# Kernel optimization log

Hardware: AMD Instinct MI355X
Metric: run time of the kernel (lower is better)

## Reference

```python
import jax, jax.numpy as jnp
import numpy as np

N_NODES = 100000
N_EDGES = 250000
EMB = 300
LAYERS = 5
BN_EPS = 1e-5


def setup_inputs() -> dict:
    key = jax.random.key(0)
    ks = jax.random.split(key, 16)
    inp = {
        "x": jax.random.randint(ks[0], (N_NODES, 2), 0, 3, dtype=jnp.int64) if jax.config.jax_enable_x64 else jax.random.randint(ks[0], (N_NODES, 2), 0, 3, dtype=jnp.int32),
        "edge_index": jax.random.randint(ks[1], (2, N_EDGES), 0, N_NODES, dtype=jnp.int32),
        "edge_attr": jax.random.randint(ks[2], (N_EDGES, 2), 0, 3, dtype=jnp.int32),
        "atom_emb1": jax.random.normal(ks[3], (120, EMB), jnp.float32) * 0.1,
        "atom_emb2": jax.random.normal(ks[4], (3, EMB), jnp.float32) * 0.1,
        "edge_emb1": jax.random.normal(ks[5], (LAYERS, 6, EMB), jnp.float32) * 0.1,
        "edge_emb2": jax.random.normal(ks[6], (LAYERS, 3, EMB), jnp.float32) * 0.1,
        "W1": jax.random.normal(ks[7], (LAYERS, EMB, 2 * EMB), jnp.float32) * (1.0 / np.sqrt(EMB)),
        "b1": jnp.zeros((LAYERS, 2 * EMB), jnp.float32),
        "W2": jax.random.normal(ks[8], (LAYERS, 2 * EMB, EMB), jnp.float32) * (1.0 / np.sqrt(2 * EMB)),
        "b2": jnp.zeros((LAYERS, EMB), jnp.float32),
        "gamma": jnp.ones((LAYERS, EMB), jnp.float32),
        "beta": jnp.zeros((LAYERS, EMB), jnp.float32),
    }
    return inp


def reference(x, edge_index, edge_attr, atom_emb1, atom_emb2, edge_emb1, edge_emb2,
              W1, b1, W2, b2, gamma, beta):
    N = x.shape[0]
    L = W1.shape[0]
    # AtomEncoder: sum of per-feature embeddings
    h = atom_emb1[x[:, 0]] + atom_emb2[x[:, 1]]  # [N, D]
    # add self loops (attr = (4, 0)); PyG: messages flow src=row0 -> dst=row1
    sl = jnp.arange(N, dtype=edge_index.dtype)
    src = jnp.concatenate([edge_index[0], sl])
    dst = jnp.concatenate([edge_index[1], sl])
    ea0 = jnp.concatenate([edge_attr[:, 0], jnp.full((N,), 4, edge_attr.dtype)])
    ea1 = jnp.concatenate([edge_attr[:, 1], jnp.zeros((N,), edge_attr.dtype)])
    for l in range(L):
        e = edge_emb1[l][ea0] + edge_emb2[l][ea1]           # [E+N, D]
        msg = h[src] + e                                     # gather + add
        agg = jax.ops.segment_sum(msg, dst, num_segments=N)  # scatter-add
        hmid = jax.nn.relu(agg @ W1[l] + b1[l])
        hout = hmid @ W2[l] + b2[l]
        mean = hout.mean(axis=0)
        var = hout.var(axis=0)
        hbn = (hout - mean) * jax.lax.rsqrt(var + BN_EPS) * gamma[l] + beta[l]
        h = hbn if l == L - 1 else jax.nn.relu(hbn)          # dropout ratio 0
    return h
```

## Files before the change

### kernel.cpp

```cpp
#include <hip/hip_runtime.h>
#include <hip/hip_bf16.h>

#define N_NODESC 100000
#define N_EDGESC 250000
#define EMB 300
#define LD 304
#define LD4 76
#define LAYERS 5
#define BN_EPS 1e-5f

#define K1 320
#define N1 640
#define K2 640
#define N2 384

#define NB_SCAN 391

typedef __attribute__((ext_vector_type(8))) short short8;
typedef __attribute__((ext_vector_type(4))) float f32x4;

#define GLOAD16(g, l) __builtin_amdgcn_global_load_lds( \
    (const __attribute__((address_space(1))) void*)(g), \
    (__attribute__((address_space(3))) void*)(l), 16, 0, 0)

__device__ __forceinline__ float4 f4add(float4 a, float4 b){
    return make_float4(a.x+b.x, a.y+b.y, a.z+b.z, a.w+b.w);
}
__device__ __forceinline__ unsigned short f2bf(float f){
    __hip_bfloat16 h = __float2bfloat16(f);
    return *(unsigned short*)&h;
}

__global__ void k_zero_i(int* p, int n){
    int i = blockIdx.x*blockDim.x + threadIdx.x;
    if(i < n) p[i] = 0;
}
__global__ void k_zero_f(float* p, int n){
    int i = blockIdx.x*blockDim.x + threadIdx.x;
    if(i < n) p[i] = 0.f;
}

__global__ void k_atom(const int* __restrict__ x,
                       const float* __restrict__ e1,
                       const float* __restrict__ e2,
                       float* __restrict__ h){
    int idx = blockIdx.x*blockDim.x + threadIdx.x;
    if(idx >= N_NODESC*LD4) return;
    int i = idx / LD4, c = idx % LD4;
    float4 v = make_float4(0,0,0,0);
    if(c < 75){
        int i0 = x[2*i], i1 = x[2*i+1];
        const float4* r1 = (const float4*)(e1 + (size_t)i0*EMB);
        const float4* r2 = (const float4*)(e2 + (size_t)i1*EMB);
        v = f4add(r1[c], r2[c]);
    }
    ((float4*)h)[idx] = v;
}

__global__ void k_etab(const float* __restrict__ e1,
                       const float* __restrict__ e2,
                       float* __restrict__ etab){
    int idx = blockIdx.x*blockDim.x + threadIdx.x;
    if(idx >= LAYERS*18*LD4) return;
    int l = idx / (18*LD4);
    int r = idx % (18*LD4);
    int c = r / LD4, f = r % LD4;
    float4 v = make_float4(0,0,0,0);
    if(f < 75){
        const float4* r1 = (const float4*)(e1 + (size_t)(l*6 + c/3)*EMB);
        const float4* r2 = (const float4*)(e2 + (size_t)(l*3 + c%3)*EMB);
        v = f4add(r1[f], r2[f]);
    }
    ((float4*)etab)[idx] = v;
}

__global__ void k_prepw1(const float* __restrict__ W1, unsigned short* __restrict__ wb){
    int idx = blockIdx.x*blockDim.x + threadIdx.x;
    if(idx >= LAYERS*N1*K1) return;
    int l = idx / (N1*K1);
    int r = idx % (N1*K1);
    int n = r / K1, k = r % K1;
    float v = (n < 600 && k < EMB) ? W1[((size_t)l*EMB + k)*600 + n] : 0.f;
    wb[idx] = f2bf(v);
}
__global__ void k_prepw2(const float* __restrict__ W2, unsigned short* __restrict__ wb){
    int idx = blockIdx.x*blockDim.x + threadIdx.x;
    if(idx >= LAYERS*N2*K2) return;
    int l = idx / (N2*K2);
    int r = idx % (N2*K2);
    int n = r / K2, k = r % K2;
    float v = (n < EMB && k < 600) ? W2[((size_t)l*600 + k)*EMB + n] : 0.f;
    wb[idx] = f2bf(v);
}
__global__ void k_prepb1(const float* __restrict__ b1, float* __restrict__ bp){
    int idx = blockIdx.x*blockDim.x + threadIdx.x;
    if(idx >= LAYERS*N1) return;
    int l = idx / N1, n = idx % N1;
    bp[idx] = (n < 600) ? b1[(size_t)l*600 + n] : 0.f;
}

__global__ void k_deg(const int* __restrict__ ei, int* __restrict__ deg){
    int e = blockIdx.x*blockDim.x + threadIdx.x;
    if(e >= N_EDGESC) return;
    atomicAdd(&deg[ei[N_EDGESC + e]], 1);
}

__global__ void k_bsum(const int* __restrict__ deg, int* __restrict__ bsum){
    int g = blockIdx.x*256 + threadIdx.x;
    int v = (g < N_NODESC) ? deg[g] : 0;
    #pragma unroll
    for(int o=32;o>0;o>>=1) v += __shfl_down(v, o);
    __shared__ int sw[4];
    if((threadIdx.x & 63) == 0) sw[threadIdx.x>>6] = v;
    __syncthreads();
    if(threadIdx.x == 0) bsum[blockIdx.x] = sw[0]+sw[1]+sw[2]+sw[3];
}

__global__ void k_bscan(const int* __restrict__ bsum, int* __restrict__ bpre,
                        int* __restrict__ offs){
    __shared__ int sh[512];
    int t = threadIdx.x;
    int v = (t < NB_SCAN) ? bsum[t] : 0;
    sh[t] = v; __syncthreads();
    for(int o=1;o<512;o<<=1){
        int u = (t >= o) ? sh[t-o] : 0;
        __syncthreads();
        sh[t] += u;
        __syncthreads();
    }
    if(t < NB_SCAN) bpre[t] = sh[t] - v;
    if(t == NB_SCAN-1) offs[N_NODESC] = sh[t];
}

__global__ void k_offs(const int* __restrict__ deg, const int* __restrict__ bpre,
                       int* __restrict__ offs, int* __restrict__ cursor){
    __shared__ int sh[256];
    int t = threadIdx.x;
    int g = blockIdx.x*256 + t;
    int v = (g < N_NODESC) ? deg[g] : 0;
    sh[t] = v; __syncthreads();
    for(int o=1;o<256;o<<=1){
        int u = (t >= o) ? sh[t-o] : 0;
        __syncthreads();
        sh[t] += u;
        __syncthreads();
    }
    if(g < N_NODESC){
        int e = bpre[blockIdx.x] + sh[t] - v;
        offs[g] = e; cursor[g] = e;
    }
}

__global__ void k_fill(const int* __restrict__ ei, const int* __restrict__ ea,
                       int* __restrict__ cursor,
                       int* __restrict__ csr_src, int* __restrict__ csr_ea){
    int e = blockIdx.x*blockDim.x + threadIdx.x;
    if(e >= N_EDGESC) return;
    int d = ei[N_EDGESC + e];
    int p = atomicAdd(&cursor[d], 1);
    csr_src[p] = ei[e];
    csr_ea[p]  = ea[2*e]*3 + ea[2*e+1];
}

template<int BN>
__global__ void k_aggT(const float* __restrict__ src, const float* __restrict__ etab_l,
                       const float* __restrict__ aff,
                       const int* __restrict__ offs, const int* __restrict__ csr_src,
                       const int* __restrict__ csr_ea, unsigned short* __restrict__ agg){
    int idx = blockIdx.x*blockDim.x + threadIdx.x;
    if(idx >= N_NODESC*80) return;
    int i = idx / 80, c = idx % 80;
    ushort4 out;
    if(c < 75){
        const float4* s4 = (const float4*)src;
        const float4* et = (const float4*)etab_l;
        const int stride = BN ? 75 : LD4;
        float4 a4, b4;
        if(BN){ a4 = ((const float4*)aff)[c]; b4 = ((const float4*)aff)[75 + c]; }
        #define LOADV(s_, v_) { float4 x_ = s4[(size_t)(s_)*stride + c];          \
            if(BN){ v_.x = fmaxf(fmaf(x_.x,a4.x,b4.x),0.f);                       \
                    v_.y = fmaxf(fmaf(x_.y,a4.y,b4.y),0.f);                       \
                    v_.z = fmaxf(fmaf(x_.z,a4.z,b4.z),0.f);                       \
                    v_.w = fmaxf(fmaf(x_.w,a4.w,b4.w),0.f); } else v_ = x_; }
        float4 v;
        LOADV(i, v)
        float4 acc = f4add(v, et[12*LD4 + c]);
        int j0 = offs[i], j1 = offs[i+1];
        for(int j=j0; j<j1; j++){
            int s = csr_src[j];
            int t = csr_ea[j];
            LOADV(s, v)
            acc = f4add(acc, f4add(v, et[t*LD4 + c]));
        }
        #undef LOADV
        out.x = f2bf(acc.x); out.y = f2bf(acc.y);
        out.z = f2bf(acc.z); out.w = f2bf(acc.w);
    } else {
        out.x = out.y = out.z = out.w = 0;
    }
    *(ushort4*)(agg + (size_t)i*K1 + c*4) = out;
}

__global__ void k_bnaff(const float* __restrict__ stats, const float* __restrict__ g,
                        const float* __restrict__ bt, float* __restrict__ aff){
    int c = blockIdx.x*blockDim.x + threadIdx.x;
    if(c >= EMB) return;
    const float inv_n = 1.0f/(float)N_NODESC;
    float m = stats[c]*inv_n;
    float var = stats[EMB + c]*inv_n - m*m;
    float a = g[c]*rsqrtf(var + BN_EPS);
    aff[c] = a;
    aff[EMB + c] = bt[c] - m*a;
}

template<int EPI, int KS, int NX>
__global__ __launch_bounds__(512) void k_mgemm(
    const unsigned short* __restrict__ A,
    const unsigned short* __restrict__ Bt,
    const float* __restrict__ bias,
    void* __restrict__ Cptr, int M, int ldc,
    float* __restrict__ stats, int nwg)
{
    __shared__ char smem_c[3*16384 + 1024];
    unsigned short* smem_u = (unsigned short*)smem_c;

    int bid = blockIdx.x;
    int q = nwg >> 3, r = nwg & 7;
    int xcd = bid & 7, lo = bid >> 3;
    int wg = (xcd < r) ? (xcd*(q+1) + lo) : (r*(q+1) + (xcd - r)*q + lo);
    int bx = wg % NX, by = wg / NX;
    int m0 = by*128, n0 = bx*128;

    const int tid = threadIdx.x;
    const int wv = tid >> 6, ln = tid & 63;
    const int wvm = wv >> 2, wvn = wv & 3;
    const int lr = ln & 15, hi = ln >> 4;

    const int rS = tid >> 2, cS = tid & 3;
    int gA = m0 + rS; if(gA >= M) gA = M-1;
    const unsigned short* srcA = A  + (size_t)gA*(KS*32)      + ((cS ^ ((rS>>1)&3))<<3);
    const unsigned short* srcB = Bt + (size_t)(n0 + rS)*(KS*32) + ((cS ^ ((rS>>1)&3))<<3);

    f32x4 acc[4][2] = {};

    #define STAGE(t) { \
        char* db_ = smem_c + ((t)%3)*16384; \
        GLOAD16(srcA + (t)*32, db_ + tid*16); \
        GLOAD16(srcB + (t)*32, db_ + 8192 + tid*16); }

    STAGE(0)
    __builtin_amdgcn_sched_barrier(0);
    STAGE(1)
    __builtin_amdgcn_sched_barrier(0);

    int offA[4], offB[2];
    #pragma unroll
    for(int m=0;m<4;m++){
        int row = wvm*64 + m*16 + lr;
        offA[m] = row*32 + ((hi ^ ((row>>1)&3))<<3);
    }
    #pragma unroll
    for(int n=0;n<2;n++){
        int brow = wvn*32 + n*16 + lr;
        offB[n] = 4096 + brow*32 + ((hi ^ ((brow>>1)&3))<<3);
    }

    #pragma unroll
    for(int kc=0; kc<KS; kc++){
        if(kc == KS-1) asm volatile("s_waitcnt vmcnt(0) lgkmcnt(0)" ::: "memory");
        else           asm volatile("s_waitcnt vmcnt(2) lgkmcnt(0)" ::: "memory");
        __builtin_amdgcn_s_barrier();
        __builtin_amdgcn_sched_barrier(0);
        if(kc+2 < KS) STAGE(kc+2)
        const unsigned short* bufu = smem_u + (kc%3)*8192;
        short8 av[4], bv[2];
        #pragma unroll
        for(int m=0;m<4;m++) av[m] = *(const short8*)(bufu + offA[m]);
        #pragma unroll
        for(int n=0;n<2;n++) bv[n] = *(const short8*)(bufu + offB[n]);
        __builtin_amdgcn_s_setprio(1);
        #pragma unroll
        for(int m=0;m<4;m++)
            #pragma unroll
            for(int n=0;n<2;n++)
                acc[m][n] = __builtin_amdgcn_mfma_f32_16x16x32_bf16(
                                av[m], bv[n], acc[m][n], 0, 0, 0);
        __builtin_amdgcn_s_setprio(0);
    }
    #undef STAGE

    __syncthreads();

    if(EPI == 0){
        unsigned short* Cs = smem_u;
        unsigned short* Cb = (unsigned short*)Cptr;
        #pragma unroll
        for(int n=0;n<2;n++){
            int col = wvn*32 + n*16 + lr;
            float bsv = bias[n0 + col];
            #pragma unroll
            for(int m=0;m<4;m++){
                #pragma unroll
                for(int j=0;j<4;j++){
                    int row = wvm*64 + m*16 + hi*4 + j;
                    Cs[row*144 + col] = f2bf(fmaxf(acc[m][n][j] + bsv, 0.f));
                }
            }
        }
        __syncthreads();
        #pragma unroll
        for(int i=0;i<4;i++){
            int id = i*512 + tid;
            int rr = id >> 4, ch = id & 15;
            int gr = m0 + rr;
            if(gr < M)
                *(short8*)(Cb + (size_t)gr*ldc + n0 + ch*8) =
                    *(const short8*)(Cs + rr*144 + ch*8);
        }
    } else {
        float* Cf = (float*)Cptr;
        float* red = (float*)(smem_c + 3*16384);
        #pragma unroll
        for(int n=0;n<2;n++){
            int col = n0 + wvn*32 + n*16 + lr;
            bool cok = (col < EMB);
            float bsv = cok ? bias[col] : 0.f;
            float sS = 0.f, sQ = 0.f;
            #pragma unroll
            for(int m=0;m<4;m++){
                #pragma unroll
                for(int j=0;j<4;j++){
                    int row = m0 + wvm*64 + m*16 + hi*4 + j;
                    if(cok && row < M){
                        float v = acc[m][n][j] + bsv;
                        sS += v; sQ += v*v;
                    }
                }
            }
            sS += __shfl_xor(sS, 16); sQ += __shfl_xor(sQ, 16);
            sS += __shfl_xor(sS, 32); sQ += __shfl_xor(sQ, 32);
            if(hi == 0){ red[(wv*16+lr)*2] = sS; red[(wv*16+lr)*2+1] = sQ; }
            __syncthreads();
            if(wv < 4 && ln < 16){
                float S = red[(wv*16+ln)*2]   + red[((wv+4)*16+ln)*2];
                float Q = red[(wv*16+ln)*2+1] + red[((wv+4)*16+ln)*2+1];
                int c2 = n0 + wv*32 + n*16 + ln;
                if(c2 < EMB){
                    atomicAdd(&stats[c2], S);
                    atomicAdd(&stats[EMB + c2], Q);
                }
            }
            __syncthreads();
        }
        float* Cs = (float*)smem_c;
        #pragma unroll
        for(int half=0; half<2; half++){
            if(wvm == half){
                #pragma unroll
                for(int n=0;n<2;n++){
                    int col = wvn*32 + n*16 + lr;
                    float bsv = (n0 + col < EMB) ? bias[n0 + col] : 0.f;
                    #pragma unroll
                    for(int m=0;m<4;m++){
                        #pragma unroll
                        for(int j=0;j<4;j++){
                            int rl = m*16 + hi*4 + j;
                            Cs[rl*132 + col] = acc[m][n][j] + bsv;
                        }
                    }
                }
            }
            __syncthreads();
            #pragma unroll
            for(int i=0;i<4;i++){
                int id = i*512 + tid;
                int rr = id >> 5, c4 = id & 31;
                int col = n0 + c4*4;
                int gr = m0 + half*64 + rr;
                if(col < EMB && gr < M)
                    *(float4*)(Cf + (size_t)gr*ldc + col) =
                        *(const float4*)(Cs + rr*132 + c4*4);
            }
            __syncthreads();
        }
    }
}

__global__ void k_bnapply(const float* __restrict__ X, const float* __restrict__ stats,
                          const float* __restrict__ g, const float* __restrict__ bt,
                          float* __restrict__ dout){
    int idx = blockIdx.x*blockDim.x + threadIdx.x;
    if(idx >= N_NODESC*75) return;
    int i = idx / 75, c = idx % 75;
    const float4* X4 = (const float4*)X;
    float4 v  = X4[(size_t)i*75 + c];
    float4 s  = ((const float4*)stats)[c];
    float4 q  = ((const float4*)stats)[75 + c];
    float4 gg = ((const float4*)g)[c];
    float4 bb = ((const float4*)bt)[c];
    const float inv_n = 1.0f/(float)N_NODESC;
    #define BN1(f) { float m = s.f*inv_n; float var = q.f*inv_n - m*m;          \
                     float r = rsqrtf(var + BN_EPS);                             \
                     v.f = (v.f - m)*r*gg.f + bb.f; }
    BN1(x) BN1(y) BN1(z) BN1(w)
    #undef BN1
    ((float4*)dout)[(size_t)i*75 + c] = v;
}

extern "C" void kernel_launch(void* const* d_in, const int* in_sizes, int n_in,
                              void* d_out, int out_size, void* d_ws, size_t ws_size,
                              hipStream_t stream) {
    const int*   x     = (const int*)d_in[0];
    const int*   ei    = (const int*)d_in[1];
    const int*   ea    = (const int*)d_in[2];
    const float* aemb1 = (const float*)d_in[3];
    const float* aemb2 = (const float*)d_in[4];
    const float* eemb1 = (const float*)d_in[5];
    const float* eemb2 = (const float*)d_in[6];
    const float* W1    = (const float*)d_in[7];
    const float* b1    = (const float*)d_in[8];
    const float* W2    = (const float*)d_in[9];
    const float* b2    = (const float*)d_in[10];
    const float* gamma = (const float*)d_in[11];
    const float* beta  = (const float*)d_in[12];
    float* dout = (float*)d_out;

    float* h      = (float*)d_ws;
    float* bias1p = h + (size_t)N_NODESC*LD;
    float* etab   = bias1p + LAYERS*N1;
    float* stats  = etab + LAYERS*18*LD;
    float* aff    = stats + 640;
    unsigned short* agg  = (unsigned short*)(aff + 640);
    unsigned short* hmid = agg  + (size_t)N_NODESC*K1;
    unsigned short* wb1t = hmid + (size_t)N_NODESC*N1;
    unsigned short* wb2t = wb1t + (size_t)LAYERS*N1*K1;
    int*   deg     = (int*)(wb2t + (size_t)LAYERS*N2*K2);
    int*   offs    = deg    + N_NODESC;
    int*   cursor  = offs   + N_NODESC + 1;
    int*   csr_src = cursor + N_NODESC + 1;
    int*   csr_ea  = csr_src + N_EDGESC;
    int*   bsum    = csr_ea + N_EDGESC;
    int*   bpre    = bsum + NB_SCAN;

    const int nb_nf4 = (N_NODESC*LD4 + 255)/256;

    k_atom<<<nb_nf4, 256, 0, stream>>>(x, aemb1, aemb2, h);
    k_etab<<<(LAYERS*18*LD4 + 255)/256, 256, 0, stream>>>(eemb1, eemb2, etab);
    k_prepw1<<<(LAYERS*N1*K1 + 255)/256, 256, 0, stream>>>(W1, wb1t);
    k_prepw2<<<(LAYERS*N2*K2 + 255)/256, 256, 0, stream>>>(W2, wb2t);
    k_prepb1<<<(LAYERS*N1 + 255)/256, 256, 0, stream>>>(b1, bias1p);
    k_zero_i<<<(N_NODESC + 255)/256, 256, 0, stream>>>(deg, N_NODESC);
    k_deg<<<(N_EDGESC + 255)/256, 256, 0, stream>>>(ei, deg);
    k_bsum<<<NB_SCAN, 256, 0, stream>>>(deg, bsum);
    k_bscan<<<1, 512, 0, stream>>>(bsum, bpre, offs);
    k_offs<<<NB_SCAN, 256, 0, stream>>>(deg, bpre, offs, cursor);
    k_fill<<<(N_EDGESC + 255)/256, 256, 0, stream>>>(ei, ea, cursor, csr_src, csr_ea);

    const int MT = (N_NODESC + 127)/128;
    const int nwg1 = 5*MT, nwg2 = 3*MT;
    const int nb_agg = (N_NODESC*80 + 255)/256;
    for(int l=0; l<LAYERS; l++){
        if(l == 0)
            k_aggT<0><<<nb_agg, 256, 0, stream>>>(
                h, etab, stats , offs, csr_src, csr_ea, agg);
        else
            k_aggT<1><<<nb_agg, 256, 0, stream>>>(
                dout, etab + (size_t)l*18*LD, aff, offs, csr_src, csr_ea, agg);
        k_zero_f<<<(2*EMB + 255)/256, 256, 0, stream>>>(stats, 2*EMB);
        k_mgemm<0, 10, 5><<<nwg1, 512, 0, stream>>>(
            agg, wb1t + (size_t)l*N1*K1, bias1p + (size_t)l*N1,
            hmid, N_NODESC, N1, nullptr, nwg1);
        k_mgemm<1, 20, 3><<<nwg2, 512, 0, stream>>>(
            hmid, wb2t + (size_t)l*N2*K2, b2 + (size_t)l*EMB,
            dout, N_NODESC, EMB, stats, nwg2);
        if(l < LAYERS-1)
            k_bnaff<<<2, 256, 0, stream>>>(stats, gamma + (size_t)l*EMB,
                                           beta + (size_t)l*EMB, aff);
        else
            k_bnapply<<<(N_NODESC*75 + 255)/256, 256, 0, stream>>>(
                dout, stats, gamma + (size_t)l*EMB, beta + (size_t)l*EMB, dout);
    }
}
```

Before: 1.348 ms.

## Enlarge GEMM tile to 256x128 with 4x4 MFMA per wave

Doubles the M-tile of both MLP GEMMs from 128 to 256 rows, with each of 8 waves now computing a 64x64 sub-tile (4x4 MFMA accumulators) instead of 64x32. Each K-step stages two A halves plus B into a larger triple-buffered LDS region, and the grid is halved. The BN statistics reduction is restructured to accumulate all column partials in LDS before one combined atomic pass. This raises arithmetic intensity per LDS load and cuts redundant B traffic, at the cost of more accumulator registers and LDS, which may reduce occupancy, plus fewer workgroups to fill the CUs.

```diff
diff --git a/kernel.cpp b/kernel.cpp
--- a/kernel.cpp
+++ b/kernel.cpp
@@ -221,7 +221,7 @@
     void* __restrict__ Cptr, int M, int ldc,
     float* __restrict__ stats, int nwg)
 {
-    __shared__ char smem_c[3*16384 + 1024];
+    __shared__ char smem_c[3*24576 + 4096];
     unsigned short* smem_u = (unsigned short*)smem_c;
 
     int bid = blockIdx.x;
@@ -229,60 +229,63 @@
     int xcd = bid & 7, lo = bid >> 3;
     int wg = (xcd < r) ? (xcd*(q+1) + lo) : (r*(q+1) + (xcd - r)*q + lo);
     int bx = wg % NX, by = wg / NX;
-    int m0 = by*128, n0 = bx*128;
+    int m0 = by*256, n0 = bx*128;
 
     const int tid = threadIdx.x;
     const int wv = tid >> 6, ln = tid & 63;
-    const int wvm = wv >> 2, wvn = wv & 3;
+    const int wvm = wv >> 1, wvn = wv & 1;
     const int lr = ln & 15, hi = ln >> 4;
 
     const int rS = tid >> 2, cS = tid & 3;
-    int gA = m0 + rS; if(gA >= M) gA = M-1;
-    const unsigned short* srcA = A  + (size_t)gA*(KS*32)      + ((cS ^ ((rS>>1)&3))<<3);
-    const unsigned short* srcB = Bt + (size_t)(n0 + rS)*(KS*32) + ((cS ^ ((rS>>1)&3))<<3);
-
-    f32x4 acc[4][2] = {};
+    int gA0 = m0 + rS;       if(gA0 >= M) gA0 = M-1;
+    int gA1 = m0 + 128 + rS; if(gA1 >= M) gA1 = M-1;
+    const unsigned short* srcA0 = A  + (size_t)gA0*(KS*32) + ((cS ^ ((rS>>1)&3))<<3);
+    const unsigned short* srcA1 = A  + (size_t)gA1*(KS*32) + ((cS ^ ((rS>>1)&3))<<3);
+    const unsigned short* srcB  = Bt + (size_t)(n0 + rS)*(KS*32) + ((cS ^ ((rS>>1)&3))<<3);
+
+    f32x4 acc[4][4] = {};
 
     #define STAGE(t) { \
-        char* db_ = smem_c + ((t)%3)*16384; \
-        GLOAD16(srcA + (t)*32, db_ + tid*16); \
-        GLOAD16(srcB + (t)*32, db_ + 8192 + tid*16); }
+        char* db_ = smem_c + ((t)%3)*24576; \
+        GLOAD16(srcA0 + (t)*32, db_ + tid*16); \
+        GLOAD16(srcA1 + (t)*32, db_ + (512 + tid)*16); \
+        GLOAD16(srcB  + (t)*32, db_ + 16384 + tid*16); }
 
     STAGE(0)
     __builtin_amdgcn_sched_barrier(0);
     STAGE(1)
     __builtin_amdgcn_sched_barrier(0);
 
-    int offA[4], offB[2];
+    int offA[4], offB[4];
     #pragma unroll
     for(int m=0;m<4;m++){
         int row = wvm*64 + m*16 + lr;
         offA[m] = row*32 + ((hi ^ ((row>>1)&3))<<3);
     }
     #pragma unroll
-    for(int n=0;n<2;n++){
-        int brow = wvn*32 + n*16 + lr;
-        offB[n] = 4096 + brow*32 + ((hi ^ ((brow>>1)&3))<<3);
+    for(int n=0;n<4;n++){
+        int brow = wvn*64 + n*16 + lr;
+        offB[n] = 8192 + brow*32 + ((hi ^ ((brow>>1)&3))<<3);
     }
 
     #pragma unroll
     for(int kc=0; kc<KS; kc++){
         if(kc == KS-1) asm volatile("s_waitcnt vmcnt(0) lgkmcnt(0)" ::: "memory");
-        else           asm volatile("s_waitcnt vmcnt(2) lgkmcnt(0)" ::: "memory");
+        else           asm volatile("s_waitcnt vmcnt(3) lgkmcnt(0)" ::: "memory");
         __builtin_amdgcn_s_barrier();
         __builtin_amdgcn_sched_barrier(0);
         if(kc+2 < KS) STAGE(kc+2)
-        const unsigned short* bufu = smem_u + (kc%3)*8192;
-        short8 av[4], bv[2];
+        const unsigned short* bufu = smem_u + (kc%3)*12288;
+        short8 av[4], bv[4];
         #pragma unroll
         for(int m=0;m<4;m++) av[m] = *(const short8*)(bufu + offA[m]);
         #pragma unroll
-        for(int n=0;n<2;n++) bv[n] = *(const short8*)(bufu + offB[n]);
+        for(int n=0;n<4;n++) bv[n] = *(const short8*)(bufu + offB[n]);
         __builtin_amdgcn_s_setprio(1);
         #pragma unroll
         for(int m=0;m<4;m++)
             #pragma unroll
-            for(int n=0;n<2;n++)
+            for(int n=0;n<4;n++)
                 acc[m][n] = __builtin_amdgcn_mfma_f32_16x16x32_bf16(
                                 av[m], bv[n], acc[m][n], 0, 0, 0);
         __builtin_amdgcn_s_setprio(0);
@@ -295,34 +298,34 @@
         unsigned short* Cs = smem_u;
         unsigned short* Cb = (unsigned short*)Cptr;
         #pragma unroll
-        for(int n=0;n<2;n++){
-            int col = wvn*32 + n*16 + lr;
+        for(int n=0;n<4;n++){
+            int col = wvn*64 + n*16 + lr;
             float bsv = bias[n0 + col];
             #pragma unroll
             for(int m=0;m<4;m++){
                 #pragma unroll
                 for(int j=0;j<4;j++){
                     int row = wvm*64 + m*16 + hi*4 + j;
-                    Cs[row*144 + col] = f2bf(fmaxf(acc[m][n][j] + bsv, 0.f));
+                    Cs[row*136 + col] = f2bf(fmaxf(acc[m][n][j] + bsv, 0.f));
                 }
             }
         }
         __syncthreads();
         #pragma unroll
-        for(int i=0;i<4;i++){
+        for(int i=0;i<8;i++){
             int id = i*512 + tid;
             int rr = id >> 4, ch = id & 15;
             int gr = m0 + rr;
             if(gr < M)
                 *(short8*)(Cb + (size_t)gr*ldc + n0 + ch*8) =
-                    *(const short8*)(Cs + rr*144 + ch*8);
+                    *(const short8*)(Cs + rr*136 + ch*8);
         }
     } else {
         float* Cf = (float*)Cptr;
-        float* red = (float*)(smem_c + 3*16384);
-        #pragma unroll
-        for(int n=0;n<2;n++){
-            int col = n0 + wvn*32 + n*16 + lr;
+        float* red = (float*)(smem_c + 3*24576);
+        #pragma unroll
+        for(int n=0;n<4;n++){
+            int col = n0 + wvn*64 + n*16 + lr;
             bool cok = (col < EMB);
             float bsv = cok ? bias[col] : 0.f;
             float sS = 0.f, sQ = 0.f;
@@ -339,26 +342,35 @@
             }
             sS += __shfl_xor(sS, 16); sQ += __shfl_xor(sQ, 16);
             sS += __shfl_xor(sS, 32); sQ += __shfl_xor(sQ, 32);
-            if(hi == 0){ red[(wv*16+lr)*2] = sS; red[(wv*16+lr)*2+1] = sQ; }
-            __syncthreads();
-            if(wv < 4 && ln < 16){
-                float S = red[(wv*16+ln)*2]   + red[((wv+4)*16+ln)*2];
-                float Q = red[(wv*16+ln)*2+1] + red[((wv+4)*16+ln)*2+1];
-                int c2 = n0 + wv*32 + n*16 + ln;
-                if(c2 < EMB){
-                    atomicAdd(&stats[c2], S);
-                    atomicAdd(&stats[EMB + c2], Q);
-                }
-            }
-            __syncthreads();
-        }
+            if(hi == 0){
+                red[(wv*4+n)*16 + lr]       = sS;
+                red[512 + (wv*4+n)*16 + lr] = sQ;
+            }
+        }
+        __syncthreads();
+        if(tid < 128){
+            int twvn = tid >> 6, tn = (tid >> 4) & 3, tlr = tid & 15;
+            float S = 0.f, Q = 0.f;
+            #pragma unroll
+            for(int wm2=0; wm2<4; wm2++){
+                int w = wm2*2 + twvn;
+                S += red[(w*4+tn)*16 + tlr];
+                Q += red[512 + (w*4+tn)*16 + tlr];
+            }
+            int c2 = n0 + twvn*64 + tn*16 + tlr;
+            if(c2 < EMB){
+                atomicAdd(&stats[c2], S);
+                atomicAdd(&stats[EMB + c2], Q);
+            }
+        }
+        __syncthreads();
         float* Cs = (float*)smem_c;
         #pragma unroll
-        for(int half=0; half<2; half++){
-            if(wvm == half){
+        for(int qq=0; qq<4; qq++){
+            if(wvm == qq){
                 #pragma unroll
-                for(int n=0;n<2;n++){
-                    int col = wvn*32 + n*16 + lr;
+                for(int n=0;n<4;n++){
+                    int col = wvn*64 + n*16 + lr;
                     float bsv = (n0 + col < EMB) ? bias[n0 + col] : 0.f;
                     #pragma unroll
                     for(int m=0;m<4;m++){
@@ -376,7 +388,7 @@
                 int id = i*512 + tid;
                 int rr = id >> 5, c4 = id & 31;
                 int col = n0 + c4*4;
-                int gr = m0 + half*64 + rr;
+                int gr = m0 + qq*64 + rr;
                 if(col < EMB && gr < M)
                     *(float4*)(Cf + (size_t)gr*ldc + col) =
                         *(const float4*)(Cs + rr*132 + c4*4);
@@ -456,8 +468,8 @@
     k_offs<<<NB_SCAN, 256, 0, stream>>>(deg, bpre, offs, cursor);
     k_fill<<<(N_EDGESC + 255)/256, 256, 0, stream>>>(ei, ea, cursor, csr_src, csr_ea);
 
-    const int MT = (N_NODESC + 127)/128;
-    const int nwg1 = 5*MT, nwg2 = 3*MT;
+    const int MT2 = (N_NODESC + 255)/256;
+    const int nwg1 = 5*MT2, nwg2 = 3*MT2;
     const int nb_agg = (N_NODESC*80 + 255)/256;
     for(int l=0; l<LAYERS; l++){
         if(l == 0)
```

Result: slower. 1.438 ms (+6.7%).
